# Kernel optimization log

Measured on AMD Instinct MI355X. Metric: run time of the kernel, lower is better.

## Reference

```python
import jax, jax.numpy as jnp
import numpy as np

B, T, D_IN = 256, 250, 700
H1, H2, D_OUT = 256, 256, 20
B_J0 = 0.01
BETA = 1.8  # adaptation strength (isAdapt=1)
LENS, SCALE, HIGHT, GAMMA = 0.5, 6.0, 0.15, 0.5
SQRT_2PI = float(np.sqrt(2.0 * np.pi))


def _gaussian(x, mu, sigma):
    return jnp.exp(-((x - mu) ** 2) / (2.0 * sigma ** 2)) / (SQRT_2PI * sigma)


@jax.custom_vjp
def act_fun(x):
    # Heaviside spike with multi-Gaussian surrogate gradient (gradient_type='MG')
    return (x > 0).astype(x.dtype)


def _act_fwd(x):
    return act_fun(x), x


def _act_bwd(x, g):
    temp = (_gaussian(x, 0.0, LENS) * (1.0 + HIGHT)
            - _gaussian(x, LENS, SCALE * LENS) * HIGHT
            - _gaussian(x, -LENS, SCALE * LENS) * HIGHT)
    return (g * temp * GAMMA,)


act_fun.defvjp(_act_fwd, _act_bwd)


def setup_inputs() -> dict:
    key = jax.random.key(0)
    ks = jax.random.split(key, 16)
    # binary-ish spike input (SHD spike trains), rand fill
    x = (jax.random.uniform(ks[0], (B, T, D_IN)) < 0.1).astype(jnp.float32)

    def xavier(k, out_d, in_d):
        lim = float(np.sqrt(6.0 / (in_d + out_d)))
        return jax.random.uniform(k, (out_d, in_d), jnp.float32, -lim, lim)

    return {
        "x": x,
        "w_i2h1": xavier(ks[1], H1, D_IN),
        "w_h12h1": xavier(ks[2], H1, H1),
        "w_h12h2": xavier(ks[3], H2, H1),
        "w_h22h2": xavier(ks[4], H2, H2),
        "w_h2o": xavier(ks[5], D_OUT, H2),
        "b_h1": jnp.zeros((H1,), jnp.float32),
        "b_h2": jnp.zeros((H2,), jnp.float32),
        "b_o": jnp.zeros((D_OUT,), jnp.float32),
        "tau_adp_h1": 150.0 + 10.0 * jax.random.normal(ks[6], (H1,), jnp.float32),
        "tau_adp_h2": 150.0 + 10.0 * jax.random.normal(ks[7], (H2,), jnp.float32),
        "tau_m_h1": 20.0 + 5.0 * jax.random.normal(ks[8], (H1,), jnp.float32),
        "tau_m_h2": 20.0 + 5.0 * jax.random.normal(ks[9], (H2,), jnp.float32),
        "tau_m_o": 20.0 + 5.0 * jax.random.normal(ks[10], (D_OUT,), jnp.float32),
    }


def _lif_step(inp, mem, spk, b, alpha, ro):
    # mem_update_adp with params=None, dparams=None, isAdapt=1, dt=1, R_m=1
    b = ro * b + BETA * (1.0 - ro) * spk
    mem = mem * alpha - b * spk + (1.0 - alpha) * inp
    spk = act_fun(mem - b - B_J0)
    return mem, spk, b


def reference(x, w_i2h1, w_h12h1, w_h12h2, w_h22h2, w_h2o,
              b_h1, b_h2, b_o, tau_adp_h1, tau_adp_h2,
              tau_m_h1, tau_m_h2, tau_m_o):
    bsz = x.shape[0]
    h1, h2, d_out = w_i2h1.shape[0], w_h12h2.shape[0], w_h2o.shape[0]

    alpha1 = jnp.exp(-1.0 / tau_m_h1)
    ro1 = jnp.exp(-1.0 / tau_adp_h1)
    alpha2 = jnp.exp(-1.0 / tau_m_h2)
    ro2 = jnp.exp(-1.0 / tau_adp_h2)
    alpha_o = jnp.exp(-1.0 / tau_m_o)

    init = (
        jnp.zeros((bsz, h1)), jnp.zeros((bsz, h1)), jnp.full((bsz, h1), B_J0),
        jnp.zeros((bsz, h2)), jnp.zeros((bsz, h2)), jnp.full((bsz, h2), B_J0),
        jnp.zeros((bsz, d_out)), jnp.zeros((bsz, d_out)),
    )
    xT = jnp.swapaxes(x, 0, 1)  # [T, B, D_in]

    def step(carry, xt):
        mem1, spk1, bb1, mem2, spk2, bb2, mem_o, acc = carry
        h1_in = xt @ w_i2h1.T + spk1 @ w_h12h1.T + b_h1
        mem1, spk1, bb1 = _lif_step(h1_in, mem1, spk1, bb1, alpha1, ro1)
        h2_in = spk1 @ w_h12h2.T + spk2 @ w_h22h2.T + b_h2
        mem2, spk2, bb2 = _lif_step(h2_in, mem2, spk2, bb2, alpha2, ro2)
        o_in = spk2 @ w_h2o.T + b_o
        mem_o = mem_o * alpha_o + (1.0 - alpha_o) * o_in  # output_Neuron
        acc = acc + jax.nn.softmax(mem_o, axis=-1)
        return (mem1, spk1, bb1, mem2, spk2, bb2, mem_o, acc), None

    carry, _ = jax.lax.scan(step, init, xT)
    return carry[-1]  # accumulated softmax over the 250 timesteps, [B, 20]
```

## Files before the change

### kernel.cpp

```cpp
#include <hip/hip_runtime.h>
#include <cstdint>
#include <cstddef>

#define BB 256
#define TT 250
#define DIN 700
#define H1 256
#define H2 256
#define DOUT 20
#define BJ0 0.01f
#define BETAC 1.8f
#define IQSCALE 3.814697265625e-06f

typedef float f32x4 __attribute__((ext_vector_type(4)));
typedef int   i32x4 __attribute__((ext_vector_type(4)));

#define COFF_BL  180224
#define SOFF_T11 180224
#define SOFF_T12 245760
#define SOFF_T22 311296
#define FOFF_W2O 188416
#define FOFF_XP  193536
#define FOFF_MO  16577536
#define N_TRANS  381952

#define BARRIER_LDS() asm volatile("s_waitcnt lgkmcnt(0)\n\ts_barrier" ::: "memory")

__device__ __forceinline__ short q18(float w) {
    float s = w * 262144.0f;
    s = fminf(fmaxf(s, -32767.0f), 32767.0f);
    return (short)__float2int_rn(s);
}

__global__ void transpose_all_k(const float* __restrict__ w_i2h1,
                                const float* __restrict__ w_h12h1,
                                const float* __restrict__ w_h12h2,
                                const float* __restrict__ w_h22h2,
                                const float* __restrict__ w_h2o,
                                signed char* __restrict__ cws,
                                short* __restrict__ sws,
                                float* __restrict__ fws) {
    int i = blockIdx.x * blockDim.x + threadIdx.x;
    if (i < 180224) {
        int h = i / 704, k = i - h * 704;
        int q = (k < DIN) ? (int)q18(w_i2h1[h * DIN + k]) : 0;
        q = q > 32639 ? 32639 : (q < -32640 ? -32640 : q);
        int hi = (q + 128) >> 8;
        int lo = q - (hi << 8);
        cws[i] = (signed char)hi;
        cws[COFF_BL + i] = (signed char)lo;
        return;
    }
    i -= 180224;
    if (i < 65536) { int d = i >> 8, h = i & 255;
        sws[SOFF_T11 + i] = q18(w_h12h1[h * H1 + d]); return; }
    i -= 65536;
    if (i < 65536) { int d = i >> 8, h = i & 255;
        sws[SOFF_T12 + i] = q18(w_h12h2[h * H1 + d]); return; }
    i -= 65536;
    if (i < 65536) { int d = i >> 8, h = i & 255;
        sws[SOFF_T22 + i] = q18(w_h22h2[h * H2 + d]); return; }
    i -= 65536;
    if (i < 5120)  { int j = i / 20, o = i % 20;
        fws[FOFF_W2O + i] = w_h2o[o * H2 + j]; return; }
}

__global__ __launch_bounds__(256) void xgemm_k(const float* __restrict__ x,
                                               const signed char* __restrict__ Bh,
                                               const signed char* __restrict__ Bl,
                                               const float* __restrict__ b_h1,
                                               float* __restrict__ Xp) {
    const int t    = threadIdx.x;
    const int lane = t & 63;
    const int w    = t >> 6;
    const int m0   = blockIdx.x * 32;

    __shared__ __align__(16) signed char Asub[32 * 720];
    __shared__ __align__(16) signed char Bhs[256 * 80];
    __shared__ __align__(16) signed char Bls[256 * 80];

    #pragma unroll
    for (int it = 0; it < 22; ++it) {
        int flat = it * 256 + t;
        int row  = flat / 176;
        int c4   = flat - row * 176;
        unsigned int pk = 0u;
        if (c4 < 175) {
            const float* xr = x + (size_t)(m0 + row) * DIN;
            float4 f = *(const float4*)(xr + (c4 << 2));
            pk = (f.x != 0.f ? 1u : 0u)
               | (f.y != 0.f ? 1u : 0u) << 8
               | (f.z != 0.f ? 1u : 0u) << 16
               | (f.w != 0.f ? 1u : 0u) << 24;
        }
        *(unsigned int*)(Asub + row * 720 + (c4 << 2)) = pk;
    }

    i32x4 acch[2][4], accl[2][4];
    #pragma unroll
    for (int mt = 0; mt < 2; ++mt)
        #pragma unroll
        for (int nt = 0; nt < 4; ++nt) {
            acch[mt][nt] = (i32x4){0, 0, 0, 0};
            accl[mt][nt] = (i32x4){0, 0, 0, 0};
        }

    const int arow  = lane & 15;
    const int kg16  = (lane >> 4) << 4;
    const int bcol0 = w << 6;

    for (int ks = 0; ks < 11; ++ks) {
        __syncthreads();
        #pragma unroll
        for (int it2 = 0; it2 < 4; ++it2) {
            int row = it2 * 64 + (t >> 2);
            int ch  = (t & 3) << 4;
            int go  = row * 704 + ks * 64 + ch;
            *(int4*)(Bhs + row * 80 + ch) = *(const int4*)(Bh + go);
            *(int4*)(Bls + row * 80 + ch) = *(const int4*)(Bl + go);
        }
        __syncthreads();

        const int ko = ks * 64 + kg16;
        i32x4 a0 = *(const i32x4*)(Asub + arow * 720 + ko);
        i32x4 a1 = *(const i32x4*)(Asub + (16 + arow) * 720 + ko);
        #pragma unroll
        for (int nt = 0; nt < 4; ++nt) {
            const int bb = (bcol0 + nt * 16 + arow) * 80 + kg16;
            i32x4 bhf = *(const i32x4*)(Bhs + bb);
            i32x4 blf = *(const i32x4*)(Bls + bb);
            acch[0][nt] = __builtin_amdgcn_mfma_i32_16x16x64_i8(a0, bhf, acch[0][nt], 0, 0, 0);
            acch[1][nt] = __builtin_amdgcn_mfma_i32_16x16x64_i8(a1, bhf, acch[1][nt], 0, 0, 0);
            accl[0][nt] = __builtin_amdgcn_mfma_i32_16x16x64_i8(a0, blf, accl[0][nt], 0, 0, 0);
            accl[1][nt] = __builtin_amdgcn_mfma_i32_16x16x64_i8(a1, blf, accl[1][nt], 0, 0, 0);
        }
    }

    const int crb = (lane >> 4) << 2;
    #pragma unroll
    for (int nt = 0; nt < 4; ++nt) {
        int col = bcol0 + nt * 16 + arow;
        float bias = b_h1[col];
        #pragma unroll
        for (int mt = 0; mt < 2; ++mt) {
            #pragma unroll
            for (int r = 0; r < 4; ++r) {
                int row = m0 + mt * 16 + crb + r;
                int ir = (acch[mt][nt][r] << 8) + accl[mt][nt][r];
                __builtin_nontemporal_store(bias + (float)ir * IQSCALE,
                                            Xp + (size_t)row * H1 + col);
            }
        }
    }
}

__device__ __forceinline__ void add8s(const short* __restrict__ T,
                                      const int* __restrict__ L, int off,
                                      int& acc) {
    int4 ea = *(const int4*)(L + off);
    int4 eb = *(const int4*)(L + off + 4);
    acc += T[ea.x << 8]; acc += T[ea.y << 8];
    acc += T[ea.z << 8]; acc += T[ea.w << 8];
    acc += T[eb.x << 8]; acc += T[eb.y << 8];
    acc += T[eb.z << 8]; acc += T[eb.w << 8];
}

__device__ __forceinline__ void tails(const short* __restrict__ T,
                                      const int* __restrict__ L, int done,
                                      int rem, int& acc) {
    if (rem >= 4) {
        int4 e = *(const int4*)(L + done);
        acc += T[e.x << 8]; acc += T[e.y << 8];
        acc += T[e.z << 8]; acc += T[e.w << 8];
        done += 4; rem -= 4;
    }
    if (rem) {
        int4 e = *(const int4*)(L + done);
        acc += T[e.x << 8];
        if (rem > 1) acc += T[e.y << 8];
        if (rem > 2) acc += T[e.z << 8];
    }
}

__device__ __forceinline__ void add8f(const float* __restrict__ T,
                                      const int* __restrict__ L, int off,
                                      float& acc) {
    int4 ea = *(const int4*)(L + off);
    int4 eb = *(const int4*)(L + off + 4);
    acc += T[ea.x * DOUT]; acc += T[ea.y * DOUT];
    acc += T[ea.z * DOUT]; acc += T[ea.w * DOUT];
    acc += T[eb.x * DOUT]; acc += T[eb.y * DOUT];
    acc += T[eb.z * DOUT]; acc += T[eb.w * DOUT];
}

__device__ __forceinline__ void tailf(const float* __restrict__ T,
                                      const int* __restrict__ L, int done,
                                      int rem, float& acc) {
    if (rem >= 4) {
        int4 e = *(const int4*)(L + done);
        acc += T[e.x * DOUT]; acc += T[e.y * DOUT];
        acc += T[e.z * DOUT]; acc += T[e.w * DOUT];
        done += 4; rem -= 4;
    }
    if (rem) {
        int4 e = *(const int4*)(L + done);
        acc += T[e.x * DOUT];
        if (rem > 1) acc += T[e.y * DOUT];
        if (rem > 2) acc += T[e.z * DOUT];
    }
}

__global__ __launch_bounds__(512) void rec_k(
    const float* __restrict__ Xp,
    const short* __restrict__ sT11, const short* __restrict__ sT12,
    const short* __restrict__ sT22, const float* __restrict__ wT2o,
    const float* __restrict__ b_h2, const float* __restrict__ b_o,
    const float* __restrict__ tau_adp_h1, const float* __restrict__ tau_adp_h2,
    const float* __restrict__ tau_m_h1, const float* __restrict__ tau_m_h2,
    const float* __restrict__ tau_m_o,
    float* __restrict__ Mo) {
    const int tid  = threadIdx.x;
    const int lane = tid & 63;
    const int w    = tid >> 6;
    const bool isL1 = (w < 4);
    const int c    = ((w & 3) << 6) + lane;
    const int b    = blockIdx.x;
    const float* __restrict__ XpB = Xp + (size_t)b * TT * H1;
    float* __restrict__ MoB = Mo + (size_t)b * TT * DOUT;

    __shared__ __align__(16) short sT22L[65536];
    __shared__ __align__(16) float w2oL[5120];
    __shared__ __align__(16) int lst1s[2][256];
    __shared__ __align__(16) int lst2s[2][256];
    __shared__ int lcnt[4][2];

    {
        const int* src = (const int*)sT22;
        int* dst = (int*)sT22L;
        for (int k = tid; k < 32768; k += 512) dst[k] = src[k];
        for (int k = tid; k < 5120; k += 512) w2oL[k] = wT2o[k];
        if (tid < 256) { lst1s[0][tid] = 0; lst1s[1][tid] = 0;
                         lst2s[0][tid] = 0; lst2s[1][tid] = 0; }
        if (tid < 8) ((int*)lcnt)[tid] = 0;
    }

    float alpha, rr, inb = 0.f;
    if (isL1) {
        alpha = expf(-1.0f / tau_m_h1[c]);
        rr    = expf(-1.0f / tau_adp_h1[c]);
    } else {
        alpha = expf(-1.0f / tau_m_h2[c]);
        rr    = expf(-1.0f / tau_adp_h2[c]);
        inb   = b_h2[c];
    }
    const int oc  = ((w & 3) * 5) + lane;
    const int ocs = (isL1 && lane < 5) ? oc : 0;
    float alpo = 0.f, bov = 0.f;
    if (isL1 && lane < 5) { alpo = expf(-1.0f / tau_m_o[oc]); bov = b_o[oc]; }

    float mem = 0.f, spk = 0.f, bbv = BJ0;
    float memo = 0.f;

    float xp_cur = 0.f;
    if (isL1) xp_cur = __builtin_nontemporal_load(XpB + c);
    __syncthreads();

    for (int i = 0; i <= TT + 1; ++i) {
        const int cur = i & 1, nxt = cur ^ 1;
        const int cc = i & 3, cn = (i + 1) & 3, cz = (i + 2) & 3;

        const int tot1 = lcnt[cc][0];
        const int tot2 = lcnt[cc][1];
        if (tid == 0) { lcnt[cz][0] = 0; lcnt[cz][1] = 0; }

        float xp_nxt = 0.f;
        if (isL1 && i + 1 < TT)
            xp_nxt = __builtin_nontemporal_load(XpB + (size_t)(i + 1) * H1 + c);

        const int* __restrict__ L1l = lst1s[cur];
        const int* __restrict__ L2l = lst2s[cur];

        int acc1 = 0, acc2 = 0;
        float ao = 0.f;

        if (isL1) {
            if (i < TT) {
                const short* colT = sT11 + c;
                int nb8 = tot1 >> 3;
                for (int kk = 0; kk < nb8; ++kk) add8s(colT, L1l, kk << 3, acc1);
                tails(colT, L1l, nb8 << 3, tot1 & 7, acc1);
            }
            if (i >= 2) {
                const float* colO = w2oL + ocs;
                int nb8 = tot2 >> 3;
                for (int kk = 0; kk < nb8; ++kk) add8f(colO, L2l, kk << 3, ao);
                tailf(colO, L2l, nb8 << 3, tot2 & 7, ao);
            }
        } else if (i >= 1 && i <= TT) {
            {
                const short* colT = sT12 + c;
                int nb8 = tot1 >> 3;
                for (int kk = 0; kk < nb8; ++kk) add8s(colT, L1l, kk << 3, acc1);
                tails(colT, L1l, nb8 << 3, tot1 & 7, acc1);
            }
            {
                const short* colL = sT22L + c;
                int nb8 = tot2 >> 3;
                for (int kk = 0; kk < nb8; ++kk) add8s(colL, L2l, kk << 3, acc2);
                tails(colL, L2l, nb8 << 3, tot2 & 7, acc2);
            }
        }

        if (isL1) {
            if (i < TT) {
                float r1 = (float)acc1 * IQSCALE;
                bbv = rr * bbv + BETAC * (1.f - rr) * spk;
                mem = mem * alpha - bbv * spk + (1.f - alpha) * (xp_cur + r1);
                float ns = (mem - bbv - BJ0) > 0.f ? 1.f : 0.f;
                spk = ns;
                unsigned long long m = __ballot(ns != 0.f ? 1 : 0);
                int base = 0;
                if (lane == 0) base = atomicAdd(&lcnt[cn][0], __popcll(m));
                base = __shfl(base, 0);
                if (ns != 0.f)
                    lst1s[nxt][base + __popcll(m & ((1ull << lane) - 1ull))] = c;
            }
            if (lane < 5 && i >= 2) {
                memo = memo * alpo + (1.f - alpo) * (bov + ao);
                __builtin_nontemporal_store(memo, MoB + (size_t)(i - 2) * DOUT + oc);
            }
        } else if (i >= 1 && i <= TT) {
            float r23 = (float)(acc1 + acc2) * IQSCALE;
            bbv = rr * bbv + BETAC * (1.f - rr) * spk;
            mem = mem * alpha - bbv * spk + (1.f - alpha) * (inb + r23);
            float ns = (mem - bbv - BJ0) > 0.f ? 1.f : 0.f;
            spk = ns;
            unsigned long long m = __ballot(ns != 0.f ? 1 : 0);
            int base = 0;
            if (lane == 0) base = atomicAdd(&lcnt[cn][1], __popcll(m));
            base = __shfl(base, 0);
            if (ns != 0.f)
                lst2s[nxt][base + __popcll(m & ((1ull << lane) - 1ull))] = c;
        }

        BARRIER_LDS();
        xp_cur = xp_nxt;
    }
}

__global__ __launch_bounds__(256) void soft_k(const float* __restrict__ Mo,
                                              float* __restrict__ out) {
    const int b = blockIdx.x;
    const int t = threadIdx.x;
    __shared__ float sm[TT][DOUT];

    if (t < TT) {
        const float* row = Mo + ((size_t)b * TT + t) * DOUT;
        float v[DOUT];
        #pragma unroll
        for (int k = 0; k < DOUT; k += 4) {
            float4 r = *(const float4*)(row + k);
            v[k] = r.x; v[k + 1] = r.y; v[k + 2] = r.z; v[k + 3] = r.w;
        }
        float mx = v[0];
        #pragma unroll
        for (int j = 1; j < DOUT; ++j) mx = fmaxf(mx, v[j]);
        float s = 0.f;
        #pragma unroll
        for (int j = 0; j < DOUT; ++j) { v[j] = __expf(v[j] - mx); s += v[j]; }
        float inv = 1.0f / s;
        #pragma unroll
        for (int j = 0; j < DOUT; ++j) sm[t][j] = v[j] * inv;
    }
    __syncthreads();
    if (t < DOUT) {
        float acc = 0.f;
        for (int tt = 0; tt < TT; ++tt) acc += sm[tt][t];
        out[b * DOUT + t] = acc;
    }
}

extern "C" void kernel_launch(void* const* d_in, const int* in_sizes, int n_in,
                              void* d_out, int out_size, void* d_ws, size_t ws_size,
                              hipStream_t stream) {
    const float* x          = (const float*)d_in[0];
    const float* w_i2h1     = (const float*)d_in[1];
    const float* w_h12h1    = (const float*)d_in[2];
    const float* w_h12h2    = (const float*)d_in[3];
    const float* w_h22h2    = (const float*)d_in[4];
    const float* w_h2o      = (const float*)d_in[5];
    const float* b_h1       = (const float*)d_in[6];
    const float* b_h2       = (const float*)d_in[7];
    const float* b_o        = (const float*)d_in[8];
    const float* tau_adp_h1 = (const float*)d_in[9];
    const float* tau_adp_h2 = (const float*)d_in[10];
    const float* tau_m_h1   = (const float*)d_in[11];
    const float* tau_m_h2   = (const float*)d_in[12];
    const float* tau_m_o    = (const float*)d_in[13];

    signed char* cws = (signed char*)d_ws;
    short* sws = (short*)d_ws;
    float* fws = (float*)d_ws;
    const signed char* Bh = cws;
    const signed char* Bl = cws + COFF_BL;
    const short* sT11 = sws + SOFF_T11;
    const short* sT12 = sws + SOFF_T12;
    const short* sT22 = sws + SOFF_T22;
    float* wT2o = fws + FOFF_W2O;
    float* Xp   = fws + FOFF_XP;
    float* Mo   = fws + FOFF_MO;

    transpose_all_k<<<N_TRANS / 256, 256, 0, stream>>>(
        w_i2h1, w_h12h1, w_h12h2, w_h22h2, w_h2o, cws, sws, fws);

    xgemm_k<<<(BB * TT) / 32, 256, 0, stream>>>(x, Bh, Bl, b_h1, Xp);

    rec_k<<<BB, 512, 0, stream>>>(Xp, sT11, sT12, sT22, wT2o,
                                  b_h2, b_o, tau_adp_h1, tau_adp_h2,
                                  tau_m_h1, tau_m_h2, tau_m_o, Mo);

    soft_k<<<BB, 256, 0, stream>>>(Mo, (float*)d_out);
}
```

Measured before the change: 684.3 us.

## Split sparse spike-gather accumulation across two wave groups per layer in rec_k

The recurrent kernel doubles its block to 1024 threads and splits each layer's sparse weight-gather loop across two 4-wave groups, interleaving the 8-element chunks between them. The second group writes its partial integer sums to LDS, and the first group adds them after a new barrier before the neuron update. The output-neuron accumulation moves to the fourth group. This is meant to shorten the serial per-timestep gather chain on the latency-bound recurrence, at the cost of an extra LDS barrier per step and tighter register limits from the larger block.

```diff
diff --git a/kernel.cpp b/kernel.cpp
--- a/kernel.cpp
+++ b/kernel.cpp
@@ -210,7 +210,7 @@
     }
 }
 
-__global__ __launch_bounds__(512) void rec_k(
+__global__ __launch_bounds__(1024, 4) void rec_k(
     const float* __restrict__ Xp,
     const short* __restrict__ sT11, const short* __restrict__ sT12,
     const short* __restrict__ sT22, const float* __restrict__ wT2o,
@@ -222,8 +222,9 @@
     const int tid  = threadIdx.x;
     const int lane = tid & 63;
     const int w    = tid >> 6;
-    const bool isL1 = (w < 4);
-    const int c    = ((w & 3) << 6) + lane;
+    const int grp  = w >> 2;
+    const int wq   = w & 3;
+    const int c    = (wq << 6) + lane;
     const int b    = blockIdx.x;
     const float* __restrict__ XpB = Xp + (size_t)b * TT * H1;
     float* __restrict__ MoB = Mo + (size_t)b * TT * DOUT;
@@ -232,37 +233,40 @@
     __shared__ __align__(16) float w2oL[5120];
     __shared__ __align__(16) int lst1s[2][256];
     __shared__ __align__(16) int lst2s[2][256];
+    __shared__ __align__(16) int pp11B[256];
+    __shared__ __align__(16) int pp12B[256];
+    __shared__ __align__(16) int pp22B[256];
     __shared__ int lcnt[4][2];
 
     {
         const int* src = (const int*)sT22;
         int* dst = (int*)sT22L;
-        for (int k = tid; k < 32768; k += 512) dst[k] = src[k];
-        for (int k = tid; k < 5120; k += 512) w2oL[k] = wT2o[k];
-        if (tid < 256) { lst1s[0][tid] = 0; lst1s[1][tid] = 0;
-                         lst2s[0][tid] = 0; lst2s[1][tid] = 0; }
+        for (int k = tid; k < 32768; k += 1024) dst[k] = src[k];
+        for (int k = tid; k < 5120; k += 1024) w2oL[k] = wT2o[k];
+        if (tid < 512) ((int*)lst1s)[tid] = 0;
+        else if (tid < 1024) ((int*)lst2s)[tid - 512] = 0;
         if (tid < 8) ((int*)lcnt)[tid] = 0;
     }
 
-    float alpha, rr, inb = 0.f;
-    if (isL1) {
+    float alpha = 0.f, rr = 0.f, inb = 0.f;
+    if (grp == 0) {
         alpha = expf(-1.0f / tau_m_h1[c]);
         rr    = expf(-1.0f / tau_adp_h1[c]);
-    } else {
+    } else if (grp == 2) {
         alpha = expf(-1.0f / tau_m_h2[c]);
         rr    = expf(-1.0f / tau_adp_h2[c]);
         inb   = b_h2[c];
     }
-    const int oc  = ((w & 3) * 5) + lane;
-    const int ocs = (isL1 && lane < 5) ? oc : 0;
+    const int oc  = wq * 5 + lane;
+    const int ocs = (grp == 3 && lane < 5) ? oc : 0;
     float alpo = 0.f, bov = 0.f;
-    if (isL1 && lane < 5) { alpo = expf(-1.0f / tau_m_o[oc]); bov = b_o[oc]; }
+    if (grp == 3 && lane < 5) { alpo = expf(-1.0f / tau_m_o[oc]); bov = b_o[oc]; }
 
     float mem = 0.f, spk = 0.f, bbv = BJ0;
     float memo = 0.f;
 
     float xp_cur = 0.f;
-    if (isL1) xp_cur = __builtin_nontemporal_load(XpB + c);
+    if (grp == 0) xp_cur = __builtin_nontemporal_load(XpB + c);
     __syncthreads();
 
     for (int i = 0; i <= TT + 1; ++i) {
@@ -274,63 +278,75 @@
         if (tid == 0) { lcnt[cz][0] = 0; lcnt[cz][1] = 0; }
 
         float xp_nxt = 0.f;
-        if (isL1 && i + 1 < TT)
+        if (grp == 0 && i + 1 < TT)
             xp_nxt = __builtin_nontemporal_load(XpB + (size_t)(i + 1) * H1 + c);
 
         const int* __restrict__ L1l = lst1s[cur];
         const int* __restrict__ L2l = lst2s[cur];
+        const int nb1 = tot1 >> 3, rem1 = tot1 & 7;
+        const int nb2 = tot2 >> 3, rem2 = tot2 & 7;
 
         int acc1 = 0, acc2 = 0;
-        float ao = 0.f;
-
-        if (isL1) {
+
+        if (grp == 0) {
             if (i < TT) {
                 const short* colT = sT11 + c;
-                int nb8 = tot1 >> 3;
-                for (int kk = 0; kk < nb8; ++kk) add8s(colT, L1l, kk << 3, acc1);
-                tails(colT, L1l, nb8 << 3, tot1 & 7, acc1);
-            }
-            if (i >= 2) {
+                for (int kk = 0; kk < nb1; kk += 2) add8s(colT, L1l, kk << 3, acc1);
+                tails(colT, L1l, nb1 << 3, rem1, acc1);
+            }
+        } else if (grp == 1) {
+            if (i < TT) {
+                const short* colT = sT11 + c;
+                for (int kk = 1; kk < nb1; kk += 2) add8s(colT, L1l, kk << 3, acc1);
+            }
+            pp11B[c] = acc1;
+        } else if (grp == 2) {
+            if (i >= 1 && i <= TT) {
+                const short* colT = sT12 + c;
+                for (int kk = 0; kk < nb1; kk += 2) add8s(colT, L1l, kk << 3, acc1);
+                tails(colT, L1l, nb1 << 3, rem1, acc1);
+                const short* colL = sT22L + c;
+                for (int kk = 0; kk < nb2; kk += 2) add8s(colL, L2l, kk << 3, acc2);
+                tails(colL, L2l, nb2 << 3, rem2, acc2);
+            }
+        } else {
+            if (i >= 1 && i <= TT) {
+                const short* colT = sT12 + c;
+                for (int kk = 1; kk < nb1; kk += 2) add8s(colT, L1l, kk << 3, acc1);
+                const short* colL = sT22L + c;
+                for (int kk = 1; kk < nb2; kk += 2) add8s(colL, L2l, kk << 3, acc2);
+            }
+            pp12B[c] = acc1;
+            pp22B[c] = acc2;
+            if (lane < 5 && i >= 2) {
+                float ao = 0.f;
                 const float* colO = w2oL + ocs;
-                int nb8 = tot2 >> 3;
-                for (int kk = 0; kk < nb8; ++kk) add8f(colO, L2l, kk << 3, ao);
-                tailf(colO, L2l, nb8 << 3, tot2 & 7, ao);
-            }
-        } else if (i >= 1 && i <= TT) {
-            {
-                const short* colT = sT12 + c;
-                int nb8 = tot1 >> 3;
-                for (int kk = 0; kk < nb8; ++kk) add8s(colT, L1l, kk << 3, acc1);
-                tails(colT, L1l, nb8 << 3, tot1 & 7, acc1);
-            }
-            {
-                const short* colL = sT22L + c;
-                int nb8 = tot2 >> 3;
-                for (int kk = 0; kk < nb8; ++kk) add8s(colL, L2l, kk << 3, acc2);
-                tails(colL, L2l, nb8 << 3, tot2 & 7, acc2);
-            }
-        }
-
-        if (isL1) {
-            if (i < TT) {
-                float r1 = (float)acc1 * IQSCALE;
-                bbv = rr * bbv + BETAC * (1.f - rr) * spk;
-                mem = mem * alpha - bbv * spk + (1.f - alpha) * (xp_cur + r1);
-                float ns = (mem - bbv - BJ0) > 0.f ? 1.f : 0.f;
-                spk = ns;
-                unsigned long long m = __ballot(ns != 0.f ? 1 : 0);
-                int base = 0;
-                if (lane == 0) base = atomicAdd(&lcnt[cn][0], __popcll(m));
-                base = __shfl(base, 0);
-                if (ns != 0.f)
-                    lst1s[nxt][base + __popcll(m & ((1ull << lane) - 1ull))] = c;
-            }
-            if (lane < 5 && i >= 2) {
+                for (int kk = 0; kk < nb2; ++kk) add8f(colO, L2l, kk << 3, ao);
+                tailf(colO, L2l, nb2 << 3, rem2, ao);
                 memo = memo * alpo + (1.f - alpo) * (bov + ao);
                 __builtin_nontemporal_store(memo, MoB + (size_t)(i - 2) * DOUT + oc);
             }
-        } else if (i >= 1 && i <= TT) {
-            float r23 = (float)(acc1 + acc2) * IQSCALE;
+        }
+
+        BARRIER_LDS();
+
+        if (grp == 0 && i < TT) {
+            int ir11 = acc1 + pp11B[c];
+            float r1 = (float)ir11 * IQSCALE;
+            bbv = rr * bbv + BETAC * (1.f - rr) * spk;
+            mem = mem * alpha - bbv * spk + (1.f - alpha) * (xp_cur + r1);
+            float ns = (mem - bbv - BJ0) > 0.f ? 1.f : 0.f;
+            spk = ns;
+            unsigned long long m = __ballot(ns != 0.f ? 1 : 0);
+            int base = 0;
+            if (lane == 0) base = atomicAdd(&lcnt[cn][0], __popcll(m));
+            base = __shfl(base, 0);
+            if (ns != 0.f)
+                lst1s[nxt][base + __popcll(m & ((1ull << lane) - 1ull))] = c;
+        } else if (grp == 2 && i >= 1 && i <= TT) {
+            int ir12 = acc1 + pp12B[c];
+            int ir22 = acc2 + pp22B[c];
+            float r23 = (float)(ir12 + ir22) * IQSCALE;
             bbv = rr * bbv + BETAC * (1.f - rr) * spk;
             mem = mem * alpha - bbv * spk + (1.f - alpha) * (inb + r23);
             float ns = (mem - bbv - BJ0) > 0.f ? 1.f : 0.f;
@@ -415,9 +431,9 @@
 
     xgemm_k<<<(BB * TT) / 32, 256, 0, stream>>>(x, Bh, Bl, b_h1, Xp);
 
-    rec_k<<<BB, 512, 0, stream>>>(Xp, sT11, sT12, sT22, wT2o,
-                                  b_h2, b_o, tau_adp_h1, tau_adp_h2,
-                                  tau_m_h1, tau_m_h2, tau_m_o, Mo);
+    rec_k<<<BB, 1024, 0, stream>>>(Xp, sT11, sT12, sT22, wT2o,
+                                   b_h2, b_o, tau_adp_h1, tau_adp_h2,
+                                   tau_m_h1, tau_m_h2, tau_m_o, Mo);
 
     soft_k<<<BB, 256, 0, stream>>>(Mo, (float*)d_out);
 }
```

Result: slower. 722.2 us (+5.5%).

## Shrink recurrent kernel to two waves, each lane owning four neurons

Applied to the files above, without the earlier changes.

The recurrent kernel drops from 512 threads (8 waves, one neuron per lane) to 128 threads (2 waves, four adjacent neurons per lane). The spike-driven weight gathers now load 4 shorts per index as one vector, and the spike lists are built by in-wave ballot prefix sums instead of LDS atomics. The 128 KB LDS copy of the layer-2 recurrent table is removed, so those reads now go to global memory/L2. This cuts barrier cost, atomics and LDS pressure per step, but each step has less parallelism and the recurrent weight reads move from LDS to cache.

```diff
diff --git a/kernel.cpp b/kernel.cpp
--- a/kernel.cpp
+++ b/kernel.cpp
@@ -13,6 +13,7 @@
 #define IQSCALE 3.814697265625e-06f
 
 typedef float f32x4 __attribute__((ext_vector_type(4)));
+typedef short s16x4 __attribute__((ext_vector_type(4)));
 typedef int   i32x4 __attribute__((ext_vector_type(4)));
 
 #define COFF_BL  180224
@@ -154,31 +155,52 @@
     }
 }
 
-__device__ __forceinline__ void add8s(const short* __restrict__ T,
+__device__ __forceinline__ void add8v(const short* __restrict__ T,
                                       const int* __restrict__ L, int off,
-                                      int& acc) {
+                                      int* a) {
     int4 ea = *(const int4*)(L + off);
     int4 eb = *(const int4*)(L + off + 4);
-    acc += T[ea.x << 8]; acc += T[ea.y << 8];
-    acc += T[ea.z << 8]; acc += T[ea.w << 8];
-    acc += T[eb.x << 8]; acc += T[eb.y << 8];
-    acc += T[eb.z << 8]; acc += T[eb.w << 8];
-}
-
-__device__ __forceinline__ void tails(const short* __restrict__ T,
+    s16x4 w0 = *(const s16x4*)(T + ((size_t)ea.x << 8));
+    s16x4 w1 = *(const s16x4*)(T + ((size_t)ea.y << 8));
+    s16x4 w2 = *(const s16x4*)(T + ((size_t)ea.z << 8));
+    s16x4 w3 = *(const s16x4*)(T + ((size_t)ea.w << 8));
+    s16x4 w4 = *(const s16x4*)(T + ((size_t)eb.x << 8));
+    s16x4 w5 = *(const s16x4*)(T + ((size_t)eb.y << 8));
+    s16x4 w6 = *(const s16x4*)(T + ((size_t)eb.z << 8));
+    s16x4 w7 = *(const s16x4*)(T + ((size_t)eb.w << 8));
+    a[0] += ((w0.x + w1.x) + (w2.x + w3.x)) + ((w4.x + w5.x) + (w6.x + w7.x));
+    a[1] += ((w0.y + w1.y) + (w2.y + w3.y)) + ((w4.y + w5.y) + (w6.y + w7.y));
+    a[2] += ((w0.z + w1.z) + (w2.z + w3.z)) + ((w4.z + w5.z) + (w6.z + w7.z));
+    a[3] += ((w0.w + w1.w) + (w2.w + w3.w)) + ((w4.w + w5.w) + (w6.w + w7.w));
+}
+
+__device__ __forceinline__ void tailv(const short* __restrict__ T,
                                       const int* __restrict__ L, int done,
-                                      int rem, int& acc) {
+                                      int rem, int* a) {
     if (rem >= 4) {
         int4 e = *(const int4*)(L + done);
-        acc += T[e.x << 8]; acc += T[e.y << 8];
-        acc += T[e.z << 8]; acc += T[e.w << 8];
+        s16x4 w0 = *(const s16x4*)(T + ((size_t)e.x << 8));
+        s16x4 w1 = *(const s16x4*)(T + ((size_t)e.y << 8));
+        s16x4 w2 = *(const s16x4*)(T + ((size_t)e.z << 8));
+        s16x4 w3 = *(const s16x4*)(T + ((size_t)e.w << 8));
+        a[0] += (w0.x + w1.x) + (w2.x + w3.x);
+        a[1] += (w0.y + w1.y) + (w2.y + w3.y);
+        a[2] += (w0.z + w1.z) + (w2.z + w3.z);
+        a[3] += (w0.w + w1.w) + (w2.w + w3.w);
         done += 4; rem -= 4;
     }
     if (rem) {
         int4 e = *(const int4*)(L + done);
-        acc += T[e.x << 8];
-        if (rem > 1) acc += T[e.y << 8];
-        if (rem > 2) acc += T[e.z << 8];
+        s16x4 w0 = *(const s16x4*)(T + ((size_t)e.x << 8));
+        a[0] += w0.x; a[1] += w0.y; a[2] += w0.z; a[3] += w0.w;
+        if (rem > 1) {
+            s16x4 w1 = *(const s16x4*)(T + ((size_t)e.y << 8));
+            a[0] += w1.x; a[1] += w1.y; a[2] += w1.z; a[3] += w1.w;
+        }
+        if (rem > 2) {
+            s16x4 w2 = *(const s16x4*)(T + ((size_t)e.z << 8));
+            a[0] += w2.x; a[1] += w2.y; a[2] += w2.z; a[3] += w2.w;
+        }
     }
 }
 
@@ -210,7 +232,7 @@
     }
 }
 
-__global__ __launch_bounds__(512) void rec_k(
+__global__ __launch_bounds__(128) void rec_k(
     const float* __restrict__ Xp,
     const short* __restrict__ sT11, const short* __restrict__ sT12,
     const short* __restrict__ sT22, const float* __restrict__ wT2o,
@@ -222,125 +244,146 @@
     const int tid  = threadIdx.x;
     const int lane = tid & 63;
     const int w    = tid >> 6;
-    const bool isL1 = (w < 4);
-    const int c    = ((w & 3) << 6) + lane;
+    const int c0   = lane << 2;
     const int b    = blockIdx.x;
     const float* __restrict__ XpB = Xp + (size_t)b * TT * H1;
     float* __restrict__ MoB = Mo + (size_t)b * TT * DOUT;
 
-    __shared__ __align__(16) short sT22L[65536];
     __shared__ __align__(16) float w2oL[5120];
     __shared__ __align__(16) int lst1s[2][256];
     __shared__ __align__(16) int lst2s[2][256];
-    __shared__ int lcnt[4][2];
-
-    {
-        const int* src = (const int*)sT22;
-        int* dst = (int*)sT22L;
-        for (int k = tid; k < 32768; k += 512) dst[k] = src[k];
-        for (int k = tid; k < 5120; k += 512) w2oL[k] = wT2o[k];
-        if (tid < 256) { lst1s[0][tid] = 0; lst1s[1][tid] = 0;
-                         lst2s[0][tid] = 0; lst2s[1][tid] = 0; }
-        if (tid < 8) ((int*)lcnt)[tid] = 0;
-    }
-
-    float alpha, rr, inb = 0.f;
-    if (isL1) {
-        alpha = expf(-1.0f / tau_m_h1[c]);
-        rr    = expf(-1.0f / tau_adp_h1[c]);
-    } else {
-        alpha = expf(-1.0f / tau_m_h2[c]);
-        rr    = expf(-1.0f / tau_adp_h2[c]);
-        inb   = b_h2[c];
-    }
-    const int oc  = ((w & 3) * 5) + lane;
-    const int ocs = (isL1 && lane < 5) ? oc : 0;
+    __shared__ int lcnt[2][2];
+
+    for (int k = tid; k < 5120; k += 128) w2oL[k] = wT2o[k];
+    for (int k = tid; k < 256; k += 128) {
+        lst1s[0][k] = 0; lst1s[1][k] = 0;
+        lst2s[0][k] = 0; lst2s[1][k] = 0;
+    }
+    if (tid < 4) ((int*)lcnt)[tid] = 0;
+
+    float alpha[4], rr[4], inb[4];
+    #pragma unroll
+    for (int s = 0; s < 4; ++s) {
+        if (w == 0) {
+            alpha[s] = expf(-1.0f / tau_m_h1[c0 + s]);
+            rr[s]    = expf(-1.0f / tau_adp_h1[c0 + s]);
+            inb[s]   = 0.f;
+        } else {
+            alpha[s] = expf(-1.0f / tau_m_h2[c0 + s]);
+            rr[s]    = expf(-1.0f / tau_adp_h2[c0 + s]);
+            inb[s]   = b_h2[c0 + s];
+        }
+    }
     float alpo = 0.f, bov = 0.f;
-    if (isL1 && lane < 5) { alpo = expf(-1.0f / tau_m_o[oc]); bov = b_o[oc]; }
-
-    float mem = 0.f, spk = 0.f, bbv = BJ0;
+    if (w == 0 && lane < DOUT) { alpo = expf(-1.0f / tau_m_o[lane]); bov = b_o[lane]; }
+
+    float mem[4] = {0.f, 0.f, 0.f, 0.f};
+    float bb[4]  = {BJ0, BJ0, BJ0, BJ0};
+    float spk[4] = {0.f, 0.f, 0.f, 0.f};
     float memo = 0.f;
 
-    float xp_cur = 0.f;
-    if (isL1) xp_cur = __builtin_nontemporal_load(XpB + c);
+    f32x4 xp_cur = (f32x4){0.f, 0.f, 0.f, 0.f};
+    if (w == 0) xp_cur = *(const f32x4*)(XpB + c0);
     __syncthreads();
 
     for (int i = 0; i <= TT + 1; ++i) {
         const int cur = i & 1, nxt = cur ^ 1;
-        const int cc = i & 3, cn = (i + 1) & 3, cz = (i + 2) & 3;
-
-        const int tot1 = lcnt[cc][0];
-        const int tot2 = lcnt[cc][1];
-        if (tid == 0) { lcnt[cz][0] = 0; lcnt[cz][1] = 0; }
-
-        float xp_nxt = 0.f;
-        if (isL1 && i + 1 < TT)
-            xp_nxt = __builtin_nontemporal_load(XpB + (size_t)(i + 1) * H1 + c);
+
+        const int tot1 = lcnt[cur][0];
+        const int tot2 = lcnt[cur][1];
+
+        f32x4 xp_nxt = (f32x4){0.f, 0.f, 0.f, 0.f};
+        if (w == 0 && i + 1 < TT)
+            xp_nxt = *(const f32x4*)(XpB + (size_t)(i + 1) * H1 + c0);
 
         const int* __restrict__ L1l = lst1s[cur];
         const int* __restrict__ L2l = lst2s[cur];
 
-        int acc1 = 0, acc2 = 0;
+        int a1[4] = {0, 0, 0, 0};
+        int a2[4] = {0, 0, 0, 0};
         float ao = 0.f;
 
-        if (isL1) {
+        if (w == 0) {
             if (i < TT) {
-                const short* colT = sT11 + c;
-                int nb8 = tot1 >> 3;
-                for (int kk = 0; kk < nb8; ++kk) add8s(colT, L1l, kk << 3, acc1);
-                tails(colT, L1l, nb8 << 3, tot1 & 7, acc1);
-            }
-            if (i >= 2) {
-                const float* colO = w2oL + ocs;
-                int nb8 = tot2 >> 3;
+                const short* colT = sT11 + c0;
+                const int nb8 = tot1 >> 3;
+                for (int kk = 0; kk < nb8; ++kk) add8v(colT, L1l, kk << 3, a1);
+                tailv(colT, L1l, nb8 << 3, tot1 & 7, a1);
+            }
+            if (lane < DOUT && i >= 2) {
+                const float* colO = w2oL + lane;
+                const int nb8 = tot2 >> 3;
                 for (int kk = 0; kk < nb8; ++kk) add8f(colO, L2l, kk << 3, ao);
                 tailf(colO, L2l, nb8 << 3, tot2 & 7, ao);
             }
         } else if (i >= 1 && i <= TT) {
-            {
-                const short* colT = sT12 + c;
-                int nb8 = tot1 >> 3;
-                for (int kk = 0; kk < nb8; ++kk) add8s(colT, L1l, kk << 3, acc1);
-                tails(colT, L1l, nb8 << 3, tot1 & 7, acc1);
-            }
-            {
-                const short* colL = sT22L + c;
-                int nb8 = tot2 >> 3;
-                for (int kk = 0; kk < nb8; ++kk) add8s(colL, L2l, kk << 3, acc2);
-                tails(colL, L2l, nb8 << 3, tot2 & 7, acc2);
-            }
-        }
-
-        if (isL1) {
+            const short* cT12 = sT12 + c0;
+            const short* cT22 = sT22 + c0;
+            const int nb81 = tot1 >> 3;
+            const int nb82 = tot2 >> 3;
+            const int nbm = nb81 > nb82 ? nb81 : nb82;
+            for (int kk = 0; kk < nbm; ++kk) {
+                if (kk < nb81) add8v(cT12, L1l, kk << 3, a1);
+                if (kk < nb82) add8v(cT22, L2l, kk << 3, a2);
+            }
+            tailv(cT12, L1l, nb81 << 3, tot1 & 7, a1);
+            tailv(cT22, L2l, nb82 << 3, tot2 & 7, a2);
+        }
+
+        if (w == 0) {
+            int tot = 0;
             if (i < TT) {
-                float r1 = (float)acc1 * IQSCALE;
-                bbv = rr * bbv + BETAC * (1.f - rr) * spk;
-                mem = mem * alpha - bbv * spk + (1.f - alpha) * (xp_cur + r1);
-                float ns = (mem - bbv - BJ0) > 0.f ? 1.f : 0.f;
-                spk = ns;
-                unsigned long long m = __ballot(ns != 0.f ? 1 : 0);
-                int base = 0;
-                if (lane == 0) base = atomicAdd(&lcnt[cn][0], __popcll(m));
-                base = __shfl(base, 0);
-                if (ns != 0.f)
-                    lst1s[nxt][base + __popcll(m & ((1ull << lane) - 1ull))] = c;
-            }
-            if (lane < 5 && i >= 2) {
+                unsigned long long Ms[4];
+                #pragma unroll
+                for (int s = 0; s < 4; ++s) {
+                    float r1 = (float)a1[s] * IQSCALE;
+                    bb[s]  = rr[s] * bb[s] + BETAC * (1.f - rr[s]) * spk[s];
+                    mem[s] = mem[s] * alpha[s] - bb[s] * spk[s]
+                           + (1.f - alpha[s]) * (xp_cur[s] + r1);
+                    float ns = (mem[s] - bb[s] - BJ0) > 0.f ? 1.f : 0.f;
+                    spk[s] = ns;
+                    Ms[s] = __ballot(ns != 0.f ? 1 : 0);
+                }
+                const unsigned long long below = (1ull << lane) - 1ull;
+                int p0 = __popcll(Ms[0]), p1 = __popcll(Ms[1]);
+                int p2 = __popcll(Ms[2]), p3 = __popcll(Ms[3]);
+                int b1 = p0, b2 = p0 + p1, b3 = p0 + p1 + p2;
+                tot = b3 + p3;
+                if (spk[0] != 0.f) lst1s[nxt][__popcll(Ms[0] & below)]      = c0;
+                if (spk[1] != 0.f) lst1s[nxt][b1 + __popcll(Ms[1] & below)] = c0 + 1;
+                if (spk[2] != 0.f) lst1s[nxt][b2 + __popcll(Ms[2] & below)] = c0 + 2;
+                if (spk[3] != 0.f) lst1s[nxt][b3 + __popcll(Ms[3] & below)] = c0 + 3;
+            }
+            if (lane == 0) lcnt[nxt][0] = tot;
+            if (lane < DOUT && i >= 2) {
                 memo = memo * alpo + (1.f - alpo) * (bov + ao);
-                __builtin_nontemporal_store(memo, MoB + (size_t)(i - 2) * DOUT + oc);
-            }
-        } else if (i >= 1 && i <= TT) {
-            float r23 = (float)(acc1 + acc2) * IQSCALE;
-            bbv = rr * bbv + BETAC * (1.f - rr) * spk;
-            mem = mem * alpha - bbv * spk + (1.f - alpha) * (inb + r23);
-            float ns = (mem - bbv - BJ0) > 0.f ? 1.f : 0.f;
-            spk = ns;
-            unsigned long long m = __ballot(ns != 0.f ? 1 : 0);
-            int base = 0;
-            if (lane == 0) base = atomicAdd(&lcnt[cn][1], __popcll(m));
-            base = __shfl(base, 0);
-            if (ns != 0.f)
-                lst2s[nxt][base + __popcll(m & ((1ull << lane) - 1ull))] = c;
+                __builtin_nontemporal_store(memo, MoB + (size_t)(i - 2) * DOUT + lane);
+            }
+        } else {
+            int tot = 0;
+            if (i >= 1 && i <= TT) {
+                unsigned long long Ms[4];
+                #pragma unroll
+                for (int s = 0; s < 4; ++s) {
+                    float r23 = (float)(a1[s] + a2[s]) * IQSCALE;
+                    bb[s]  = rr[s] * bb[s] + BETAC * (1.f - rr[s]) * spk[s];
+                    mem[s] = mem[s] * alpha[s] - bb[s] * spk[s]
+                           + (1.f - alpha[s]) * (inb[s] + r23);
+                    float ns = (mem[s] - bb[s] - BJ0) > 0.f ? 1.f : 0.f;
+                    spk[s] = ns;
+                    Ms[s] = __ballot(ns != 0.f ? 1 : 0);
+                }
+                const unsigned long long below = (1ull << lane) - 1ull;
+                int p0 = __popcll(Ms[0]), p1 = __popcll(Ms[1]);
+                int p2 = __popcll(Ms[2]), p3 = __popcll(Ms[3]);
+                int b1 = p0, b2 = p0 + p1, b3 = p0 + p1 + p2;
+                tot = b3 + p3;
+                if (spk[0] != 0.f) lst2s[nxt][__popcll(Ms[0] & below)]      = c0;
+                if (spk[1] != 0.f) lst2s[nxt][b1 + __popcll(Ms[1] & below)] = c0 + 1;
+                if (spk[2] != 0.f) lst2s[nxt][b2 + __popcll(Ms[2] & below)] = c0 + 2;
+                if (spk[3] != 0.f) lst2s[nxt][b3 + __popcll(Ms[3] & below)] = c0 + 3;
+            }
+            if (lane == 0) lcnt[nxt][1] = tot;
         }
 
         BARRIER_LDS();
@@ -415,7 +458,7 @@
 
     xgemm_k<<<(BB * TT) / 32, 256, 0, stream>>>(x, Bh, Bl, b_h1, Xp);
 
-    rec_k<<<BB, 512, 0, stream>>>(Xp, sT11, sT12, sT22, wT2o,
+    rec_k<<<BB, 128, 0, stream>>>(Xp, sT11, sT12, sT22, wT2o,
                                   b_h2, b_o, tau_adp_h1, tau_adp_h2,
                                   tau_m_h1, tau_m_h2, tau_m_o, Mo);
 
```

Result: slower. 753.5 us (+10.1%).
